# Kernel optimization log

Hardware: AMD Instinct MI355X
Metric: run time of the kernel (lower is better)

Reference implementation:

```python
import jax, jax.numpy as jnp
import numpy as np

B, D = 65536, 1024
E, U, T = 10, 10, 2  # experts, expert units, tasks


def setup_inputs() -> dict:
    key = jax.random.key(0)
    ks = jax.random.split(key, 8)
    s = 0.02
    return {
        "x": jax.random.normal(ks[0], (B, D), dtype=jnp.float32),
        "show_index": jax.random.randint(ks[1], (B,), 0, 100),
        "st": jax.random.normal(ks[2], (B, 16), dtype=jnp.float32),
        "expert_w": jax.random.normal(ks[3], (E, D, U), dtype=jnp.float32) * s,
        "expert_b": jnp.zeros((E, U), dtype=jnp.float32),
        "gate_w": jax.random.normal(ks[4], (T, D, E), dtype=jnp.float32) * s,
        "gate_b": jnp.zeros((T, E), dtype=jnp.float32),
        "ctr_w": jax.random.normal(ks[5], (U, 1), dtype=jnp.float32) * s,
        "ctr_b": jnp.zeros((1,), dtype=jnp.float32),
        "cvr_w": jax.random.normal(ks[6], (U, 1), dtype=jnp.float32) * s,
        "cvr_b": jnp.zeros((1,), dtype=jnp.float32),
    }


def reference(x, show_index, st, expert_w, expert_b, gate_w, gate_b,
              ctr_w, ctr_b, cvr_w, cvr_b):
    # experts_output[b, u, e] = relu(x @ W_e + b_e)  (stacked on axis 2)
    experts_output = jax.nn.relu(
        jnp.einsum("bd,edu->bue", x, expert_w) + expert_b.T[None, :, :]
    )  # [B, U, E]
    # gates[b, t, e] = softmax over experts
    gates = jax.nn.softmax(
        jnp.einsum("bd,tde->bte", x, gate_w) + gate_b[None, :, :], axis=-1
    )  # [B, T, E]
    # weighted sum over experts for each task: [B, T, U]
    task_inputs = jnp.einsum("bue,bte->btu", experts_output, gates)
    ctr_logits = jax.nn.sigmoid(task_inputs[:, 0, :] @ ctr_w + ctr_b)  # [B, 1]
    cvr_logits = jax.nn.sigmoid(task_inputs[:, 1, :] @ cvr_w + cvr_b)  # [B, 1]
    return (ctr_logits, cvr_logits)
```

## Files before the change

### kernel.cpp

```cpp
#include <hip/hip_runtime.h>

#define B_ROWS 65536
#define D_DIM  1024
#define NC     120
#define MBLK   64
#define BK     64
#define CSTR   121

typedef __attribute__((ext_vector_type(4))) float f32x4;
typedef __attribute__((ext_vector_type(8))) short bf16x8;

__device__ __attribute__((aligned(16))) short g_wt[128 * D_DIM];

__device__ __forceinline__ unsigned short f2bf(float f) {
  union { float f; unsigned u; } v; v.f = f;
  unsigned r = v.u + 0x7FFFu + ((v.u >> 16) & 1u);
  return (unsigned short)(r >> 16);
}

__device__ __forceinline__ bf16x8 cvt8(float4 p, float4 q) {
  bf16x8 r;
  r[0] = (short)f2bf(p.x); r[1] = (short)f2bf(p.y);
  r[2] = (short)f2bf(p.z); r[3] = (short)f2bf(p.w);
  r[4] = (short)f2bf(q.x); r[5] = (short)f2bf(q.y);
  r[6] = (short)f2bf(q.z); r[7] = (short)f2bf(q.w);
  return r;
}

__global__ __launch_bounds__(256) void pack_w(const float* __restrict__ ew,
                                              const float* __restrict__ gw) {
  int idx = blockIdx.x * 256 + threadIdx.x;
  int c = idx >> 10, d = idx & 1023;
  float v = 0.f;
  if (c < 100) {
    int e = c / 10, u = c % 10;
    v = ew[(e * D_DIM + d) * 10 + u];
  } else if (c < NC) {
    int q = c - 100; int t = q / 10, e = q % 10;
    v = gw[(t * D_DIM + d) * 10 + e];
  }
  g_wt[c * D_DIM + (d ^ ((c & 7) << 3))] = (short)f2bf(v);
}

union __align__(16) Smem {
  struct { short B0[128 * 64]; short B1[128 * 64]; } s;
  float C[MBLK * CSTR];
};

typedef const __attribute__((address_space(1))) void as1_cvoid;
typedef __attribute__((address_space(3))) void as3_void;

__device__ __forceinline__ void gload_lds16(const void* g, void* l) {
  __builtin_amdgcn_global_load_lds((as1_cvoid*)g, (as3_void*)l, 16, 0, 0);
}

__global__ __launch_bounds__(256, 4) void mmoe_main(
    const float* __restrict__ x,
    const float* __restrict__ eb, const float* __restrict__ gb,
    const float* __restrict__ ctr_w, const float* __restrict__ ctr_b,
    const float* __restrict__ cvr_w, const float* __restrict__ cvr_b,
    float* __restrict__ out) {
  __shared__ Smem sm;
  const int tid  = threadIdx.x;
  const int wave = tid >> 6, lane = tid & 63;
  const int lhi  = lane >> 4, llo = lane & 15;
  const int m0   = blockIdx.x * MBLK;
  const int bswz = (llo & 7) << 3;

  const float* ax = x + (size_t)(m0 + wave * 16 + llo) * D_DIM + lhi * 8;

  const short* bsrc = g_wt + (lane >> 3) * D_DIM + (lane & 7) * 8;
  short* const b0p = sm.s.B0 + wave * 2048 + lane * 8;
  short* const b1p = sm.s.B1 + wave * 2048 + lane * 8;

  f32x4 acc[8];
  #pragma unroll
  for (int i = 0; i < 8; ++i) acc[i] = (f32x4){0.f, 0.f, 0.f, 0.f};
  float4 a0[4], a1[4];

#define STAGE0(K0) do { _Pragma("unroll") \
    for (int j = 0; j < 4; ++j) \
      gload_lds16(bsrc + (wave * 4 + j) * 8 * D_DIM + (K0), b0p + j * 512); \
  } while (0)
#define STAGE1(K0) do { _Pragma("unroll") \
    for (int j = 0; j < 4; ++j) \
      gload_lds16(bsrc + (wave * 4 + j) * 8 * D_DIM + (K0), b1p + j * 512); \
  } while (0)
#define LOADA(AR, K0) do { \
    AR[0] = *reinterpret_cast<const float4*>(ax + (K0)); \
    AR[1] = *reinterpret_cast<const float4*>(ax + (K0) + 4); \
    AR[2] = *reinterpret_cast<const float4*>(ax + (K0) + 32); \
    AR[3] = *reinterpret_cast<const float4*>(ax + (K0) + 36); \
  } while (0)
#define COMPUTE(BUF, AR) do { \
    const bf16x8 af0 = cvt8(AR[0], AR[1]); \
    const bf16x8 af1 = cvt8(AR[2], AR[3]); \
    _Pragma("unroll") \
    for (int ct = 0; ct < 8; ++ct) { \
      const bf16x8 b = *reinterpret_cast<const bf16x8*>( \
          (BUF) + (ct * 16 + llo) * 64 + ((lhi * 8) ^ bswz)); \
      acc[ct] = __builtin_amdgcn_mfma_f32_16x16x32_bf16(af0, b, acc[ct], 0, 0, 0); \
    } \
    _Pragma("unroll") \
    for (int ct = 0; ct < 8; ++ct) { \
      const bf16x8 b = *reinterpret_cast<const bf16x8*>( \
          (BUF) + (ct * 16 + llo) * 64 + ((32 + lhi * 8) ^ bswz)); \
      acc[ct] = __builtin_amdgcn_mfma_f32_16x16x32_bf16(af1, b, acc[ct], 0, 0, 0); \
    } \
  } while (0)

  STAGE0(0);
  LOADA(a0, 0);
  __syncthreads();

  #pragma unroll
  for (int tt = 0; tt < 8; ++tt) {
    const int t = 2 * tt;
    LOADA(a1, (t + 1) * BK);
    STAGE1((t + 1) * BK);
    COMPUTE(sm.s.B0, a0);
    __syncthreads();
    if (tt < 7) {
      LOADA(a0, (t + 2) * BK);
      STAGE0((t + 2) * BK);
    }
    COMPUTE(sm.s.B1, a1);
    __syncthreads();
  }

  #pragma unroll
  for (int ct = 0; ct < 8; ++ct) {
    const int col = ct * 16 + llo;
    if (col < NC) {
      #pragma unroll
      for (int r = 0; r < 4; ++r)
        sm.C[(wave * 16 + lhi * 4 + r) * CSTR + col] = acc[ct][r];
    }
  }
  __syncthreads();

  if (tid < 2 * MBLK) {
    const int task = tid >> 6, row = tid & 63;
    const float* crow = &sm.C[row * CSTR];
    const float* wv = task ? cvr_w : ctr_w;
    const float  bv = task ? cvr_b[0] : ctr_b[0];
    float w[10];
    #pragma unroll
    for (int u = 0; u < 10; ++u) w[u] = wv[u];
    float s[10];
    #pragma unroll
    for (int e = 0; e < 10; ++e) {
      float a = 0.f;
      #pragma unroll
      for (int u = 0; u < 10; ++u) {
        float v = fmaxf(crow[e * 10 + u] + eb[e * 10 + u], 0.f);
        a = fmaf(v, w[u], a);
      }
      s[e] = a;
    }
    float gl[10], mx = -1e30f;
    #pragma unroll
    for (int e = 0; e < 10; ++e) {
      gl[e] = crow[100 + task * 10 + e] + gb[task * 10 + e];
      mx = fmaxf(mx, gl[e]);
    }
    float den = 0.f, num = 0.f;
    #pragma unroll
    for (int e = 0; e < 10; ++e) {
      float p = __expf(gl[e] - mx);
      den += p; num = fmaf(p, s[e], num);
    }
    float z = num / den + bv;
    out[task * B_ROWS + m0 + row] = 1.f / (1.f + __expf(-z));
  }
}

extern "C" void kernel_launch(void* const* d_in, const int* in_sizes, int n_in,
                              void* d_out, int out_size, void* d_ws, size_t ws_size,
                              hipStream_t stream) {
  const float* x     = (const float*)d_in[0];
  const float* ew    = (const float*)d_in[3];
  const float* eb    = (const float*)d_in[4];
  const float* gw    = (const float*)d_in[5];
  const float* gb    = (const float*)d_in[6];
  const float* ctr_w = (const float*)d_in[7];
  const float* ctr_b = (const float*)d_in[8];
  const float* cvr_w = (const float*)d_in[9];
  const float* cvr_b = (const float*)d_in[10];
  float* out = (float*)d_out;
  (void)d_ws; (void)ws_size;

  pack_w<<<512, 256, 0, stream>>>(ew, gw);
  mmoe_main<<<B_ROWS / MBLK, 256, 0, stream>>>(x, eb, gb, ctr_w, ctr_b,
                                               cvr_w, cvr_b, out);
}
```

Measured before the change: 395.0 us.

## Read packed weights directly from global memory instead of LDS staging

Removes the double-buffered LDS staging of the bf16 weight tile, including the global_load_lds path, the XOR swizzle and the per-step barriers. Each wave now loads its B fragments straight from global memory, relying on the small 240KB packed weight array staying cache-resident. The fixed software pipeline is replaced by a simple loop, and the launch-bounds occupancy hint is dropped. This saves LDS and synchronisation cost, but risks exposed global latency with no prefetch of A or B and redundant weight loads from all four waves.

```diff
diff --git a/kernel.cpp b/kernel.cpp
--- a/kernel.cpp
+++ b/kernel.cpp
@@ -4,7 +4,6 @@
 #define D_DIM  1024
 #define NC     120
 #define MBLK   64
-#define BK     64
 #define CSTR   121
 
 typedef __attribute__((ext_vector_type(4))) float f32x4;
@@ -39,93 +38,56 @@
     int q = c - 100; int t = q / 10, e = q % 10;
     v = gw[(t * D_DIM + d) * 10 + e];
   }
-  g_wt[c * D_DIM + (d ^ ((c & 7) << 3))] = (short)f2bf(v);
+  g_wt[c * D_DIM + d] = (short)f2bf(v);
 }
 
-union __align__(16) Smem {
-  struct { short B0[128 * 64]; short B1[128 * 64]; } s;
-  float C[MBLK * CSTR];
-};
-
-typedef const __attribute__((address_space(1))) void as1_cvoid;
-typedef __attribute__((address_space(3))) void as3_void;
-
-__device__ __forceinline__ void gload_lds16(const void* g, void* l) {
-  __builtin_amdgcn_global_load_lds((as1_cvoid*)g, (as3_void*)l, 16, 0, 0);
-}
-
-__global__ __launch_bounds__(256, 4) void mmoe_main(
+__global__ __launch_bounds__(256) void mmoe_main(
     const float* __restrict__ x,
     const float* __restrict__ eb, const float* __restrict__ gb,
     const float* __restrict__ ctr_w, const float* __restrict__ ctr_b,
     const float* __restrict__ cvr_w, const float* __restrict__ cvr_b,
     float* __restrict__ out) {
-  __shared__ Smem sm;
+  __shared__ float Cs[MBLK * CSTR];
   const int tid  = threadIdx.x;
   const int wave = tid >> 6, lane = tid & 63;
   const int lhi  = lane >> 4, llo = lane & 15;
   const int m0   = blockIdx.x * MBLK;
-  const int bswz = (llo & 7) << 3;
 
   const float* ax = x + (size_t)(m0 + wave * 16 + llo) * D_DIM + lhi * 8;
 
-  const short* bsrc = g_wt + (lane >> 3) * D_DIM + (lane & 7) * 8;
-  short* const b0p = sm.s.B0 + wave * 2048 + lane * 8;
-  short* const b1p = sm.s.B1 + wave * 2048 + lane * 8;
+  const short* bp[8];
+  #pragma unroll
+  for (int ct = 0; ct < 8; ++ct)
+    bp[ct] = g_wt + (ct * 16 + llo) * D_DIM + lhi * 8;
 
   f32x4 acc[8];
   #pragma unroll
   for (int i = 0; i < 8; ++i) acc[i] = (f32x4){0.f, 0.f, 0.f, 0.f};
-  float4 a0[4], a1[4];
 
-#define STAGE0(K0) do { _Pragma("unroll") \
-    for (int j = 0; j < 4; ++j) \
-      gload_lds16(bsrc + (wave * 4 + j) * 8 * D_DIM + (K0), b0p + j * 512); \
-  } while (0)
-#define STAGE1(K0) do { _Pragma("unroll") \
-    for (int j = 0; j < 4; ++j) \
-      gload_lds16(bsrc + (wave * 4 + j) * 8 * D_DIM + (K0), b1p + j * 512); \
-  } while (0)
-#define LOADA(AR, K0) do { \
-    AR[0] = *reinterpret_cast<const float4*>(ax + (K0)); \
-    AR[1] = *reinterpret_cast<const float4*>(ax + (K0) + 4); \
-    AR[2] = *reinterpret_cast<const float4*>(ax + (K0) + 32); \
-    AR[3] = *reinterpret_cast<const float4*>(ax + (K0) + 36); \
-  } while (0)
-#define COMPUTE(BUF, AR) do { \
-    const bf16x8 af0 = cvt8(AR[0], AR[1]); \
-    const bf16x8 af1 = cvt8(AR[2], AR[3]); \
-    _Pragma("unroll") \
-    for (int ct = 0; ct < 8; ++ct) { \
-      const bf16x8 b = *reinterpret_cast<const bf16x8*>( \
-          (BUF) + (ct * 16 + llo) * 64 + ((lhi * 8) ^ bswz)); \
-      acc[ct] = __builtin_amdgcn_mfma_f32_16x16x32_bf16(af0, b, acc[ct], 0, 0, 0); \
-    } \
-    _Pragma("unroll") \
-    for (int ct = 0; ct < 8; ++ct) { \
-      const bf16x8 b = *reinterpret_cast<const bf16x8*>( \
-          (BUF) + (ct * 16 + llo) * 64 + ((32 + lhi * 8) ^ bswz)); \
-      acc[ct] = __builtin_amdgcn_mfma_f32_16x16x32_bf16(af1, b, acc[ct], 0, 0, 0); \
-    } \
-  } while (0)
-
-  STAGE0(0);
-  LOADA(a0, 0);
-  __syncthreads();
-
-  #pragma unroll
-  for (int tt = 0; tt < 8; ++tt) {
-    const int t = 2 * tt;
-    LOADA(a1, (t + 1) * BK);
-    STAGE1((t + 1) * BK);
-    COMPUTE(sm.s.B0, a0);
-    __syncthreads();
-    if (tt < 7) {
-      LOADA(a0, (t + 2) * BK);
-      STAGE0((t + 2) * BK);
+  for (int cc = 0; cc < 4; ++cc) {
+    #pragma unroll
+    for (int q = 0; q < 4; ++q) {
+      const int k0 = q * 64;
+      const float4 A0 = *reinterpret_cast<const float4*>(ax + k0);
+      const float4 A1 = *reinterpret_cast<const float4*>(ax + k0 + 4);
+      const float4 A2 = *reinterpret_cast<const float4*>(ax + k0 + 32);
+      const float4 A3 = *reinterpret_cast<const float4*>(ax + k0 + 36);
+      const bf16x8 af0 = cvt8(A0, A1);
+      const bf16x8 af1 = cvt8(A2, A3);
+      #pragma unroll
+      for (int ct = 0; ct < 8; ++ct) {
+        const bf16x8 bb = *reinterpret_cast<const bf16x8*>(bp[ct] + k0);
+        acc[ct] = __builtin_amdgcn_mfma_f32_16x16x32_bf16(af0, bb, acc[ct], 0, 0, 0);
+      }
+      #pragma unroll
+      for (int ct = 0; ct < 8; ++ct) {
+        const bf16x8 bb = *reinterpret_cast<const bf16x8*>(bp[ct] + k0 + 32);
+        acc[ct] = __builtin_amdgcn_mfma_f32_16x16x32_bf16(af1, bb, acc[ct], 0, 0, 0);
+      }
     }
-    COMPUTE(sm.s.B1, a1);
-    __syncthreads();
+    ax += 256;
+    #pragma unroll
+    for (int ct = 0; ct < 8; ++ct) bp[ct] += 256;
   }
 
   #pragma unroll
@@ -134,14 +96,14 @@
     if (col < NC) {
       #pragma unroll
       for (int r = 0; r < 4; ++r)
-        sm.C[(wave * 16 + lhi * 4 + r) * CSTR + col] = acc[ct][r];
+        Cs[(wave * 16 + lhi * 4 + r) * CSTR + col] = acc[ct][r];
     }
   }
   __syncthreads();
 
   if (tid < 2 * MBLK) {
     const int task = tid >> 6, row = tid & 63;
-    const float* crow = &sm.C[row * CSTR];
+    const float* crow = &Cs[row * CSTR];
     const float* wv = task ? cvr_w : ctr_w;
     const float  bv = task ? cvr_b[0] : ctr_b[0];
     float w[10];
```

New measurement: 465.0 us. +17.7%, slower.
